# Kernel tuning notes

Hardware: AMD Instinct MI355X
Metric: run time of the kernel (lower is better)

## Reference

```python
import jax, jax.numpy as jnp
import numpy as np

HEADS = 8


def _gat(X, A, Wq, Wk, Wv, Wo, units):
    B, N, _ = X.shape
    # QKV projections -> [B, H, N, units]
    Q = (X @ Wq).reshape(B, N, HEADS, units).transpose(0, 2, 1, 3)
    K = (X @ Wk).reshape(B, N, HEADS, units).transpose(0, 2, 1, 3)
    V = (X @ Wv).reshape(B, N, HEADS, units).transpose(0, 2, 1, 3)
    scores = jnp.einsum('bhnd,bhmd->bhnm', Q, K) / jnp.sqrt(jnp.float32(units))
    # source adds A * -1e9 (masks where A == 1)
    scores = scores + A[:, None, :, :] * (-1e9)
    w = jax.nn.softmax(scores, axis=-1)  # dropout off at inference
    ctx = jnp.einsum('bhnm,bhmd->bhnd', w, V)
    ctx = ctx.transpose(0, 2, 1, 3).reshape(B, N, HEADS * units)
    return ctx @ Wo


def setup_inputs() -> dict:
    key = jax.random.key(0)
    ks = jax.random.split(key, 16)
    B, N, F = 8, 1024, 64
    u1, u2 = 128, 64
    g = lambda k, s: (jax.random.normal(k, s, dtype=jnp.float32)
                      * np.sqrt(2.0 / (s[0] + s[-1])).astype(np.float32))
    X = jax.random.normal(ks[0], (B, N, F), dtype=jnp.float32)
    A = jax.random.bernoulli(ks[1], 0.5, (B, N, N)).astype(jnp.float32)
    return {
        'X': X, 'A': A,
        'Wq1': g(ks[2], (F, u1 * HEADS)), 'Wk1': g(ks[3], (F, u1 * HEADS)),
        'Wv1': g(ks[4], (F, u1 * HEADS)), 'Wo1': g(ks[5], (u1 * HEADS, u1)),
        'Wq2': g(ks[6], (u1, u2 * HEADS)), 'Wk2': g(ks[7], (u1, u2 * HEADS)),
        'Wv2': g(ks[8], (u1, u2 * HEADS)), 'Wo2': g(ks[9], (u2 * HEADS, u2)),
        'W1': g(ks[10], (u2, 32)), 'b1': jnp.zeros((32,), jnp.float32),
        'W2': g(ks[11], (32, 16)), 'b2': jnp.zeros((16,), jnp.float32),
        'W3': g(ks[12], (16, 1)), 'b3': jnp.zeros((1,), jnp.float32),
    }


def reference(X, A, Wq1, Wk1, Wv1, Wo1, Wq2, Wk2, Wv2, Wo2,
              W1, b1, W2, b2, W3, b3):
    h = _gat(X, A, Wq1, Wk1, Wv1, Wo1, 128)   # [B, N, 128]
    h = _gat(h, A, Wq2, Wk2, Wv2, Wo2, 64)    # [B, N, 64]
    h = jnp.mean(h, axis=1)                   # [B, 64]
    h = jax.nn.relu(h @ W1 + b1)
    h = jax.nn.relu(h @ W2 + b2)
    return h @ W3 + b3                        # [B, 1]
```

## Files before the change

kernel.cpp:

```cpp
#include <hip/hip_runtime.h>
#include <hip/hip_bf16.h>
#include <math.h>

#define NB 8
#define NN 1024
#define NH 8

typedef __attribute__((ext_vector_type(8))) short bf16x8;
typedef __attribute__((ext_vector_type(4))) float f32x4;
typedef unsigned int u32;
typedef unsigned short u16;

__device__ __forceinline__ u16 f2bf(float f) {
    union { float f; u32 u; } v; v.f = f;
    const u32 u = v.u;
    return (u16)((u + 0x7fffu + ((u >> 16) & 1u)) >> 16);
}

__device__ __forceinline__ u32 cvt_pk_bf16(float lo, float hi) {
    u32 r;
    asm("v_cvt_pk_bf16_f32 %0, %1, %2" : "=v"(r) : "v"(lo), "v"(hi));
    return r;
}

__global__ __launch_bounds__(256) void mask_bits(const float* __restrict__ A,
                                                 u32* __restrict__ bits) {
    const int row = blockIdx.x;
    const int tid = threadIdx.x;
    const int lane = tid & 63;
    const float* __restrict__ ar = A + (size_t)row * NN;
#pragma unroll
    for (int it = 0; it < 4; ++it) {
        const int i = it * 256 + tid;
        const unsigned long long bal = __ballot(ar[i] != 0.0f);
        const int w0 = (it * 256 + (tid & ~63)) >> 5;
        if (lane == 0)  bits[(size_t)row * 32 + w0]     = (u32)bal;
        if (lane == 32) bits[(size_t)row * 32 + w0 + 1] = (u32)(bal >> 32);
    }
}

__global__ __launch_bounds__(256)
void cvt_bf16(const float* __restrict__ in, u16* __restrict__ out) {
    const int i = blockIdx.x * 256 + threadIdx.x;
    const float4 a = ((const float4*)in)[2 * i];
    const float4 b = ((const float4*)in)[2 * i + 1];
    u16 t[8] = {f2bf(a.x), f2bf(a.y), f2bf(a.z), f2bf(a.w),
                f2bf(b.x), f2bf(b.y), f2bf(b.z), f2bf(b.w)};
    ((uint4*)out)[i] = *(uint4*)t;
}

template <int KIN, int HD>
__global__ __launch_bounds__(256)
void cvt_qkvT(const float* __restrict__ Wq, const float* __restrict__ Wk,
              const float* __restrict__ Wv, u16* __restrict__ WT) {
    const int idx = blockIdx.x * 256 + threadIdx.x;
    const int c  = idx / (KIN / 8);
    const int f0 = (idx % (KIN / 8)) * 8;
    const float* __restrict__ W = (c < HD) ? Wq : (c < 2 * HD) ? Wk : Wv;
    const int cc = c % HD;
    u16 tmp[8];
#pragma unroll
    for (int j = 0; j < 8; ++j)
        tmp[j] = f2bf(W[(size_t)(f0 + j) * HD + cc]);
    *(uint4*)&WT[(size_t)c * KIN + f0] = *(uint4*)tmp;
}

template <int CIN, int COUT>
__global__ __launch_bounds__(256)
void cvt_woT(const float* __restrict__ Wo, u16* __restrict__ WoT) {
    const int idx = blockIdx.x * 256 + threadIdx.x;
    const int n  = idx / (CIN / 8);
    const int k0 = (idx % (CIN / 8)) * 8;
    u16 tmp[8];
#pragma unroll
    for (int j = 0; j < 8; ++j)
        tmp[j] = f2bf(Wo[(size_t)(k0 + j) * COUT + n]);
    *(uint4*)&WoT[(size_t)n * CIN + k0] = *(uint4*)tmp;
}

template <int KIN, int HD, int D>
__global__ __launch_bounds__(256)
void proj_mfma(const u16* __restrict__ Xb,
               const u16* __restrict__ WT,
               u16* __restrict__ Qb,
               u16* __restrict__ Kb,
               u16* __restrict__ VT,
               const float qscale) {
    constexpr int NKT = KIN / 32;
    constexpr int NTW = (3 * HD / 16) / 4;

    const int tid  = threadIdx.x;
    const int w    = tid >> 6;
    const int lane = tid & 63;
    const int g    = lane >> 4;
    const int q16  = lane & 15;
    const int r0   = blockIdx.x * 16;
    const int b    = r0 >> 10;
    const int n0   = r0 & 1023;
    const int ch   = n0 >> 5;
    const int grp  = (n0 >> 4) & 1;

    bf16x8 af[NKT];
#pragma unroll
    for (int t = 0; t < NKT; ++t)
        af[t] = *(const bf16x8*)&Xb[(size_t)(r0 + q16) * KIN + t * 32 + g * 8];

#pragma unroll 1
    for (int i = 0; i < NTW; ++i) {
        const int nt = w + 4 * i;
        const int c0 = nt * 16;
        f32x4 acc = (f32x4)0.f;
#pragma unroll
        for (int t = 0; t < NKT; ++t) {
            const bf16x8 wf = *(const bf16x8*)&WT[(size_t)(c0 + q16) * KIN + t * 32 + g * 8];
            acc = __builtin_amdgcn_mfma_f32_16x16x32_bf16(af[t], wf, acc, 0, 0, 0);
        }

        const int wcl = c0 / HD;
        const int cc  = c0 % HD;
        const int h   = cc / D;
        const int d0  = cc % D;
        const int bh  = b * NH + h;

        if (wcl == 2) {
            u16 tmp[4];
#pragma unroll
            for (int r = 0; r < 4; ++r) tmp[r] = f2bf(acc[r]);
            *(uint2*)&VT[(((size_t)bh * 32 + ch) * D + d0 + q16) * 32
                         + 8 * g + 4 * grp] = *(uint2*)tmp;
        } else {
            u16* __restrict__ O = wcl ? Kb : Qb;
            const float sc = wcl ? 1.0f : qscale;
#pragma unroll
            for (int r = 0; r < 4; ++r)
                O[((size_t)bh * NN + n0 + 4 * g + r) * D + d0 + q16] = f2bf(acc[r] * sc);
        }
    }
}

template <int D>
__global__ __launch_bounds__(256, 2)
void attn_v10(const u16* __restrict__ Qb,
              const u16* __restrict__ Kb,
              const u16* __restrict__ VT,
              const u32* __restrict__ bits,
              u16* __restrict__ Ob) {
    constexpr int ND4 = D / 32;
    constexpr int NDT = D / 16;
    constexpr int KROWB = 2 * D;
    constexpr int KBYTES = 32 * KROWB;
    constexpr int VBYTES = D * 80;

    const int tid  = threadIdx.x;
    const int w    = tid >> 6;
    const int lane = tid & 63;
    const int g    = lane >> 4;
    const int q16  = lane & 15;

    const int xcd    = blockIdx.x & 7;
    const int within = blockIdx.x >> 3;
    const int bh     = xcd * 8 + (within >> 3);
    const int b      = bh >> 3, h = bh & 7;
    const int q0     = ((within & 7) * 4 + w) * 32;

    const u16* __restrict__ qbase = Qb + (size_t)bh * NN * D;
    const u16* __restrict__ kbase = Kb + (size_t)bh * NN * D;
    const u16* __restrict__ vbase = VT + (size_t)bh * 32 * D * 32;
    const u32* __restrict__ brow0 = bits + ((size_t)b * NN + q0 + q16) * 32;
    const u32* __restrict__ brow1 = brow0 + 16 * 32;

    __shared__ alignas(16) char KsB[2][KBYTES];
    __shared__ alignas(16) char VsB[2][VBYTES];

    bool doK, doV;
    int kRow = 0, kA = 0, vD = 0, vHalf = 0;
    if constexpr (D == 128) {
        doK = true; doV = true;
        kRow = tid >> 3; kA = tid & 7;
        vD = tid >> 1;  vHalf = tid & 1;
    } else {
        doK = (tid < 128); doV = !doK;
        kRow = tid >> 2; kA = tid & 3;
        const int vt = tid - 128;
        vD = vt >> 1;   vHalf = vt & 1;
    }

    bf16x8 qf[2][ND4];
#pragma unroll
    for (int qs = 0; qs < 2; ++qs)
#pragma unroll
        for (int f = 0; f < ND4; ++f)
            qf[qs][f] = *(const bf16x8*)
                &qbase[(size_t)(q0 + qs * 16 + q16) * D + f * 32 + g * 8];

    f32x4 acc[2][NDT];
#pragma unroll
    for (int qs = 0; qs < 2; ++qs)
#pragma unroll
        for (int dt = 0; dt < NDT; ++dt) acc[qs][dt] = (f32x4)0.f;
    float l0 = 0.f, l1 = 0.f;

    uint4 sk0, sk1, sv0, sv1;
    auto stage_load = [&](int ch) {
        if (doK) {
            const u16* src = kbase + (size_t)(ch * 32 + kRow) * D + kA * 16;
            sk0 = *(const uint4*)(src);
            sk1 = *(const uint4*)(src + 8);
        }
        if (doV) {
            const u16* src = vbase + ((size_t)ch * D + vD) * 32 + vHalf * 16;
            sv0 = *(const uint4*)(src);
            sv1 = *(const uint4*)(src + 8);
        }
    };
    auto stage_write = [&](int buf) {
        if (doK) {
            char* kr = KsB[buf] + kRow * KROWB;
            *(uint4*)(kr + (((2 * kA)     ^ (kRow & 7)) * 16)) = sk0;
            *(uint4*)(kr + (((2 * kA + 1) ^ (kRow & 7)) * 16)) = sk1;
        }
        if (doV) {
            char* vr = VsB[buf] + vD * 80 + vHalf * 32;
            *(uint4*)(vr)      = sv0;
            *(uint4*)(vr + 16) = sv1;
        }
    };

    stage_load(0);
    stage_write(0);
    stage_load(1);
    __syncthreads();

#pragma unroll 1
    for (int ch = 0; ch < 32; ++ch) {
        const int cur = ch & 1;
        if (ch + 1 < 32) stage_write(cur ^ 1);
        if (ch + 2 < 32) stage_load(ch + 2);

        const u32 bw0 = brow0[ch];
        const u32 bw1 = brow1[ch];

        bf16x8 kf[2][ND4];
#pragma unroll
        for (int kb = 0; kb < 2; ++kb)
#pragma unroll
            for (int f = 0; f < ND4; ++f)
                kf[kb][f] = *(const bf16x8*)
                    (KsB[cur] + (kb * 16 + q16) * KROWB + (((f * 4 + g) ^ (q16 & 7)) * 16));

        f32x4 sA0 = (f32x4)0.f, sA1 = (f32x4)0.f;
        f32x4 sB0 = (f32x4)0.f, sB1 = (f32x4)0.f;
#pragma unroll
        for (int f = 0; f < ND4; ++f) {
            sA0 = __builtin_amdgcn_mfma_f32_16x16x32_bf16(kf[0][f], qf[0][f], sA0, 0, 0, 0);
            sA1 = __builtin_amdgcn_mfma_f32_16x16x32_bf16(kf[1][f], qf[0][f], sA1, 0, 0, 0);
            sB0 = __builtin_amdgcn_mfma_f32_16x16x32_bf16(kf[0][f], qf[1][f], sB0, 0, 0, 0);
            sB1 = __builtin_amdgcn_mfma_f32_16x16x32_bf16(kf[1][f], qf[1][f], sB1, 0, 0, 0);
        }

        bf16x8 vf[NDT];
#pragma unroll
        for (int dt = 0; dt < NDT; ++dt)
            vf[dt] = *(const bf16x8*)(VsB[cur] + (dt * 16 + q16) * 80 + g * 16);

        const u32 sh0 = bw0 >> (g * 4);
        const u32 sh1 = bw1 >> (g * 4);
        float pA0[4], pA1[4], pB0[4], pB1[4];
#pragma unroll
        for (int r = 0; r < 4; ++r) {
            const float eA0 = exp2f(sA0[r]), eA1 = exp2f(sA1[r]);
            const float eB0 = exp2f(sB0[r]), eB1 = exp2f(sB1[r]);
            pA0[r] = ((sh0 >> r) & 1u)        ? 0.f : eA0;
            pA1[r] = ((sh0 >> (16 + r)) & 1u) ? 0.f : eA1;
            pB0[r] = ((sh1 >> r) & 1u)        ? 0.f : eB0;
            pB1[r] = ((sh1 >> (16 + r)) & 1u) ? 0.f : eB1;
        }
        l0 += ((pA0[0] + pA0[1]) + (pA0[2] + pA0[3]))
            + ((pA1[0] + pA1[1]) + (pA1[2] + pA1[3]));
        l1 += ((pB0[0] + pB0[1]) + (pB0[2] + pB0[3]))
            + ((pB1[0] + pB1[1]) + (pB1[2] + pB1[3]));

        union { u32 u[4]; bf16x8 v; } paA, paB;
        paA.u[0] = cvt_pk_bf16(pA0[0], pA0[1]);
        paA.u[1] = cvt_pk_bf16(pA0[2], pA0[3]);
        paA.u[2] = cvt_pk_bf16(pA1[0], pA1[1]);
        paA.u[3] = cvt_pk_bf16(pA1[2], pA1[3]);
        paB.u[0] = cvt_pk_bf16(pB0[0], pB0[1]);
        paB.u[1] = cvt_pk_bf16(pB0[2], pB0[3]);
        paB.u[2] = cvt_pk_bf16(pB1[0], pB1[1]);
        paB.u[3] = cvt_pk_bf16(pB1[2], pB1[3]);

#pragma unroll
        for (int dt = 0; dt < NDT; ++dt) {
            acc[0][dt] = __builtin_amdgcn_mfma_f32_16x16x32_bf16(paA.v, vf[dt], acc[0][dt], 0, 0, 0);
            acc[1][dt] = __builtin_amdgcn_mfma_f32_16x16x32_bf16(paB.v, vf[dt], acc[1][dt], 0, 0, 0);
        }

        __syncthreads();
    }

#pragma unroll
    for (int qs = 0; qs < 2; ++qs) {
        float l = qs ? l1 : l0;
        l += __shfl_xor(l, 16);
        l += __shfl_xor(l, 32);
        const float inv = 1.0f / l;
        float ivr[4];
#pragma unroll
        for (int r = 0; r < 4; ++r) ivr[r] = __shfl(inv, g * 4 + r);
#pragma unroll
        for (int dt = 0; dt < NDT; ++dt)
#pragma unroll
            for (int r = 0; r < 4; ++r) {
                const int q = q0 + qs * 16 + g * 4 + r;
                Ob[(((size_t)b * NN + q) * NH + h) * D + dt * 16 + q16] =
                    f2bf(acc[qs][dt][r] * ivr[r]);
            }
    }
}

template <int CIN, int COUT, bool BF16OUT>
__global__ __launch_bounds__(256)
void wo_mfma(const u16* __restrict__ ctxb,
             const u16* __restrict__ WoT,
             void* __restrict__ Hout) {
    constexpr int NTW = COUT / 64;
    const int tid  = threadIdx.x;
    const int w    = tid >> 6;
    const int lane = tid & 63;
    const int g    = lane >> 4;
    const int q16  = lane & 15;
    const int r0   = blockIdx.x * 16;

    f32x4 acc[NTW];
#pragma unroll
    for (int nt = 0; nt < NTW; ++nt) acc[nt] = (f32x4)0.f;

    const u16* __restrict__ arow = ctxb + (size_t)(r0 + q16) * CIN + g * 8;

#pragma unroll 4
    for (int k0 = 0; k0 < CIN; k0 += 32) {
        const bf16x8 af = *(const bf16x8*)(arow + k0);
#pragma unroll
        for (int nt = 0; nt < NTW; ++nt) {
            const int n = (w * NTW + nt) * 16 + q16;
            const bf16x8 wf = *(const bf16x8*)&WoT[(size_t)n * CIN + k0 + g * 8];
            acc[nt] = __builtin_amdgcn_mfma_f32_16x16x32_bf16(af, wf, acc[nt], 0, 0, 0);
        }
    }

#pragma unroll
    for (int nt = 0; nt < NTW; ++nt)
#pragma unroll
        for (int r = 0; r < 4; ++r) {
            const size_t off = (size_t)(r0 + 4 * g + r) * COUT + (w * NTW + nt) * 16 + q16;
            if constexpr (BF16OUT) ((u16*)Hout)[off] = f2bf(acc[nt][r]);
            else                   ((float*)Hout)[off] = acc[nt][r];
        }
}

__global__ __launch_bounds__(256)
void pool_partial(const float* __restrict__ H2, float* __restrict__ partial) {
    const int b  = blockIdx.x >> 5;
    const int ch = blockIdx.x & 31;
    const int tid = threadIdx.x;
    const int o = tid & 63;
    const int g = tid >> 6;

    __shared__ float red[4][64];
    float acc = 0.f;
#pragma unroll
    for (int i = 0; i < 8; ++i) {
        const int n = ch * 32 + g * 8 + i;
        acc += H2[((size_t)b * NN + n) * 64 + o];
    }
    red[g][o] = acc;
    __syncthreads();
    if (g == 0)
        partial[((size_t)b * 32 + ch) * 64 + o] =
            (red[0][o] + red[1][o]) + (red[2][o] + red[3][o]);
}

__global__ __launch_bounds__(256)
void pool_mlp2(const float* __restrict__ partial,
               const float* __restrict__ W1, const float* __restrict__ b1,
               const float* __restrict__ W2, const float* __restrict__ b2,
               const float* __restrict__ W3, const float* __restrict__ b3,
               float* __restrict__ out) {
    const int b = blockIdx.x;
    const int tid = threadIdx.x;
    const int o = tid & 63;
    const int g = tid >> 6;
    __shared__ float red[4][64];
    __shared__ float mean[64];
    __shared__ float h1[32];
    __shared__ float h2[16];

    float acc = 0.f;
#pragma unroll
    for (int c = 0; c < 8; ++c)
        acc += partial[((size_t)b * 32 + g * 8 + c) * 64 + o];
    red[g][o] = acc;
    __syncthreads();
    if (g == 0)
        mean[o] = ((red[0][o] + red[1][o]) + (red[2][o] + red[3][o])) * (1.0f / 1024.0f);
    __syncthreads();

    if (tid < 32) {
        float a = b1[tid];
#pragma unroll
        for (int f = 0; f < 64; ++f) a = fmaf(mean[f], W1[f * 32 + tid], a);
        h1[tid] = fmaxf(a, 0.f);
    }
    __syncthreads();
    if (tid < 16) {
        float a = b2[tid];
#pragma unroll
        for (int f = 0; f < 32; ++f) a = fmaf(h1[f], W2[f * 16 + tid], a);
        h2[tid] = fmaxf(a, 0.f);
    }
    __syncthreads();
    if (tid == 0) {
        float a = b3[0];
#pragma unroll
        for (int f = 0; f < 16; ++f) a = fmaf(h2[f], W3[f], a);
        out[b] = a;
    }
}

extern "C" void kernel_launch(void* const* d_in, const int* in_sizes, int n_in,
                              void* d_out, int out_size, void* d_ws, size_t ws_size,
                              hipStream_t stream) {
    const float* X   = (const float*)d_in[0];
    const float* A   = (const float*)d_in[1];
    const float* Wq1 = (const float*)d_in[2];
    const float* Wk1 = (const float*)d_in[3];
    const float* Wv1 = (const float*)d_in[4];
    const float* Wo1 = (const float*)d_in[5];
    const float* Wq2 = (const float*)d_in[6];
    const float* Wk2 = (const float*)d_in[7];
    const float* Wv2 = (const float*)d_in[8];
    const float* Wo2 = (const float*)d_in[9];
    const float* W1  = (const float*)d_in[10];
    const float* b1  = (const float*)d_in[11];
    const float* W2  = (const float*)d_in[12];
    const float* b2  = (const float*)d_in[13];
    const float* W3  = (const float*)d_in[14];
    const float* b3  = (const float*)d_in[15];
    float* out = (float*)d_out;

    u32* bits   = (u32*)d_ws;
    u16* base   = (u16*)(bits + 262144);
    u16* Qb1    = base;  base += 8388608;
    u16* Kb1    = base;  base += 8388608;
    u16* VT1    = base;  base += 8388608;
    u16* ctx1b  = base;  base += 8388608;
    u16* WoT1   = base;  base += 131072;
    u16* Qb2    = base;  base += 4194304;
    u16* Kb2    = base;  base += 4194304;
    u16* VT2    = base;  base += 4194304;
    u16* ctx2b  = base;  base += 4194304;
    u16* WoT2   = base;  base += 32768;
    u16* Xb     = base;  base += 524288;
    u16* WqkvT1 = base;  base += 196608;
    u16* WqkvT2 = base;  base += 196608;
    u16* H1b    = base;  base += 1048576;
    float* H2   = (float*)base;
    float* partial = H2 + 524288;

    const int ROWS = NB * NN;
    const float LOG2E = 1.4426950408889634f;

    mask_bits<<<ROWS, 256, 0, stream>>>(A, bits);
    cvt_bf16<<<ROWS * 64 / 8 / 256, 256, 0, stream>>>(X, Xb);
    cvt_qkvT<64, 1024><<<3072 * 64 / 8 / 256, 256, 0, stream>>>(Wq1, Wk1, Wv1, WqkvT1);
    cvt_qkvT<128, 512><<<1536 * 128 / 8 / 256, 256, 0, stream>>>(Wq2, Wk2, Wv2, WqkvT2);
    cvt_woT<1024, 128><<<128 * 1024 / 8 / 256, 256, 0, stream>>>(Wo1, WoT1);
    cvt_woT<512, 64><<<64 * 512 / 8 / 256, 256, 0, stream>>>(Wo2, WoT2);

    proj_mfma<64, 1024, 128><<<ROWS / 16, 256, 0, stream>>>(
        Xb, WqkvT1, Qb1, Kb1, VT1, 0.08838834764831845f * LOG2E);
    attn_v10<128><<<512, 256, 0, stream>>>(Qb1, Kb1, VT1, bits, ctx1b);
    wo_mfma<1024, 128, true><<<ROWS / 16, 256, 0, stream>>>(ctx1b, WoT1, H1b);

    proj_mfma<128, 512, 64><<<ROWS / 16, 256, 0, stream>>>(
        H1b, WqkvT2, Qb2, Kb2, VT2, 0.125f * LOG2E);
    attn_v10<64><<<512, 256, 0, stream>>>(Qb2, Kb2, VT2, bits, ctx2b);
    wo_mfma<512, 64, false><<<ROWS / 16, 256, 0, stream>>>(ctx2b, WoT2, H2);

    pool_partial<<<256, 256, 0, stream>>>(H2, partial);
    pool_mlp2<<<NB, 256, 0, stream>>>(partial, W1, b1, W2, b2, W3, b3, out);
}
```

Baseline: 218.8 us.

## Widen attention key chunk to 64, compute row sums via MFMA, add setprio

Each attention loop iteration now processes 64 keys instead of 32, halving the iteration and barrier count and doubling the LDS staging buffers. The softmax denominator is accumulated with an extra MFMA against a vector of ones, which replaces the scalar adds and the final cross-lane shuffles. The MFMA phases are wrapped in s_setprio to favour matrix issue across waves. The larger LDS footprint and higher register pressure may reduce occupancy under the two-blocks-per-CU launch bound. Summing bf16-rounded probabilities also changes numerics slightly.

```diff
diff --git a/kernel.cpp b/kernel.cpp
--- a/kernel.cpp
+++ b/kernel.cpp
@@ -140,7 +140,7 @@
 
 template <int D>
 __global__ __launch_bounds__(256, 2)
-void attn_v10(const u16* __restrict__ Qb,
+void attn_v11(const u16* __restrict__ Qb,
               const u16* __restrict__ Kb,
               const u16* __restrict__ VT,
               const u32* __restrict__ bits,
@@ -148,8 +148,9 @@
     constexpr int ND4 = D / 32;
     constexpr int NDT = D / 16;
     constexpr int KROWB = 2 * D;
-    constexpr int KBYTES = 32 * KROWB;
-    constexpr int VBYTES = D * 80;
+    constexpr int KBYTES = 64 * KROWB;
+    constexpr int VROWB = 144;
+    constexpr int VBYTES = D * VROWB;
 
     const int tid  = threadIdx.x;
     const int w    = tid >> 6;
@@ -173,16 +174,15 @@
     __shared__ alignas(16) char VsB[2][VBYTES];
 
     bool doK, doV;
-    int kRow = 0, kA = 0, vD = 0, vHalf = 0;
+    int kRow = 0, kU0 = 0, vD = 0, vHalf = 0;
     if constexpr (D == 128) {
         doK = true; doV = true;
-        kRow = tid >> 3; kA = tid & 7;
-        vD = tid >> 1;  vHalf = tid & 1;
+        kRow = tid >> 2;           kU0 = (tid & 3) * 4;
+        vD   = tid >> 1;           vHalf = tid & 1;
     } else {
         doK = (tid < 128); doV = !doK;
-        kRow = tid >> 2; kA = tid & 3;
-        const int vt = tid - 128;
-        vD = vt >> 1;   vHalf = vt & 1;
+        kRow = (tid & 127) >> 1;   kU0 = (tid & 1) * 4;
+        vD   = (tid & 127) >> 1;   vHalf = tid & 1;
     }
 
     bf16x8 qf[2][ND4];
@@ -194,35 +194,48 @@
                 &qbase[(size_t)(q0 + qs * 16 + q16) * D + f * 32 + g * 8];
 
     f32x4 acc[2][NDT];
-#pragma unroll
-    for (int qs = 0; qs < 2; ++qs)
+    f32x4 accL[2];
+#pragma unroll
+    for (int qs = 0; qs < 2; ++qs) {
+        accL[qs] = (f32x4)0.f;
 #pragma unroll
         for (int dt = 0; dt < NDT; ++dt) acc[qs][dt] = (f32x4)0.f;
-    float l0 = 0.f, l1 = 0.f;
-
-    uint4 sk0, sk1, sv0, sv1;
+    }
+
+    const short oneb = (short)0x3F80;
+    const bf16x8 ones = {oneb, oneb, oneb, oneb, oneb, oneb, oneb, oneb};
+
+    uint4 skr0, skr1, skr2, skr3, svr0, svr1, svr2, svr3;
     auto stage_load = [&](int ch) {
         if (doK) {
-            const u16* src = kbase + (size_t)(ch * 32 + kRow) * D + kA * 16;
-            sk0 = *(const uint4*)(src);
-            sk1 = *(const uint4*)(src + 8);
+            const u16* src = kbase + (size_t)(ch * 64 + kRow) * D + kU0 * 8;
+            skr0 = *(const uint4*)(src);
+            skr1 = *(const uint4*)(src + 8);
+            skr2 = *(const uint4*)(src + 16);
+            skr3 = *(const uint4*)(src + 24);
         }
         if (doV) {
-            const u16* src = vbase + ((size_t)ch * D + vD) * 32 + vHalf * 16;
-            sv0 = *(const uint4*)(src);
-            sv1 = *(const uint4*)(src + 8);
+            const u16* src = vbase + ((size_t)(ch * 2 + vHalf) * D + vD) * 32;
+            svr0 = *(const uint4*)(src);
+            svr1 = *(const uint4*)(src + 8);
+            svr2 = *(const uint4*)(src + 16);
+            svr3 = *(const uint4*)(src + 24);
         }
     };
     auto stage_write = [&](int buf) {
         if (doK) {
             char* kr = KsB[buf] + kRow * KROWB;
-            *(uint4*)(kr + (((2 * kA)     ^ (kRow & 7)) * 16)) = sk0;
-            *(uint4*)(kr + (((2 * kA + 1) ^ (kRow & 7)) * 16)) = sk1;
+            *(uint4*)(kr + (((kU0 + 0) ^ (kRow & 7)) * 16)) = skr0;
+            *(uint4*)(kr + (((kU0 + 1) ^ (kRow & 7)) * 16)) = skr1;
+            *(uint4*)(kr + (((kU0 + 2) ^ (kRow & 7)) * 16)) = skr2;
+            *(uint4*)(kr + (((kU0 + 3) ^ (kRow & 7)) * 16)) = skr3;
         }
         if (doV) {
-            char* vr = VsB[buf] + vD * 80 + vHalf * 32;
-            *(uint4*)(vr)      = sv0;
-            *(uint4*)(vr + 16) = sv1;
+            char* vr = VsB[buf] + vD * VROWB + vHalf * 64;
+            *(uint4*)(vr)      = svr0;
+            *(uint4*)(vr + 16) = svr1;
+            *(uint4*)(vr + 32) = svr2;
+            *(uint4*)(vr + 48) = svr3;
         }
     };
 
@@ -232,82 +245,84 @@
     __syncthreads();
 
 #pragma unroll 1
-    for (int ch = 0; ch < 32; ++ch) {
+    for (int ch = 0; ch < 16; ++ch) {
         const int cur = ch & 1;
-        if (ch + 1 < 32) stage_write(cur ^ 1);
-        if (ch + 2 < 32) stage_load(ch + 2);
-
-        const u32 bw0 = brow0[ch];
-        const u32 bw1 = brow1[ch];
-
-        bf16x8 kf[2][ND4];
-#pragma unroll
-        for (int kb = 0; kb < 2; ++kb)
+        if (ch + 1 < 16) stage_write(cur ^ 1);
+        if (ch + 2 < 16) stage_load(ch + 2);
+
+        const uint2 bwA = *(const uint2*)(brow0 + ch * 2);
+        const uint2 bwB = *(const uint2*)(brow1 + ch * 2);
+
+        f32x4 s[2][4];
+#pragma unroll
+        for (int qs = 0; qs < 2; ++qs)
+#pragma unroll
+            for (int kb = 0; kb < 4; ++kb) s[qs][kb] = (f32x4)0.f;
+
+        __builtin_amdgcn_s_setprio(1);
+#pragma unroll
+        for (int kb = 0; kb < 4; ++kb) {
+            bf16x8 kf[ND4];
 #pragma unroll
             for (int f = 0; f < ND4; ++f)
-                kf[kb][f] = *(const bf16x8*)
+                kf[f] = *(const bf16x8*)
                     (KsB[cur] + (kb * 16 + q16) * KROWB + (((f * 4 + g) ^ (q16 & 7)) * 16));
-
-        f32x4 sA0 = (f32x4)0.f, sA1 = (f32x4)0.f;
-        f32x4 sB0 = (f32x4)0.f, sB1 = (f32x4)0.f;
-#pragma unroll
-        for (int f = 0; f < ND4; ++f) {
-            sA0 = __builtin_amdgcn_mfma_f32_16x16x32_bf16(kf[0][f], qf[0][f], sA0, 0, 0, 0);
-            sA1 = __builtin_amdgcn_mfma_f32_16x16x32_bf16(kf[1][f], qf[0][f], sA1, 0, 0, 0);
-            sB0 = __builtin_amdgcn_mfma_f32_16x16x32_bf16(kf[0][f], qf[1][f], sB0, 0, 0, 0);
-            sB1 = __builtin_amdgcn_mfma_f32_16x16x32_bf16(kf[1][f], qf[1][f], sB1, 0, 0, 0);
-        }
-
-        bf16x8 vf[NDT];
-#pragma unroll
-        for (int dt = 0; dt < NDT; ++dt)
-            vf[dt] = *(const bf16x8*)(VsB[cur] + (dt * 16 + q16) * 80 + g * 16);
-
-        const u32 sh0 = bw0 >> (g * 4);
-        const u32 sh1 = bw1 >> (g * 4);
-        float pA0[4], pA1[4], pB0[4], pB1[4];
-#pragma unroll
-        for (int r = 0; r < 4; ++r) {
-            const float eA0 = exp2f(sA0[r]), eA1 = exp2f(sA1[r]);
-            const float eB0 = exp2f(sB0[r]), eB1 = exp2f(sB1[r]);
-            pA0[r] = ((sh0 >> r) & 1u)        ? 0.f : eA0;
-            pA1[r] = ((sh0 >> (16 + r)) & 1u) ? 0.f : eA1;
-            pB0[r] = ((sh1 >> r) & 1u)        ? 0.f : eB0;
-            pB1[r] = ((sh1 >> (16 + r)) & 1u) ? 0.f : eB1;
-        }
-        l0 += ((pA0[0] + pA0[1]) + (pA0[2] + pA0[3]))
-            + ((pA1[0] + pA1[1]) + (pA1[2] + pA1[3]));
-        l1 += ((pB0[0] + pB0[1]) + (pB0[2] + pB0[3]))
-            + ((pB1[0] + pB1[1]) + (pB1[2] + pB1[3]));
-
-        union { u32 u[4]; bf16x8 v; } paA, paB;
-        paA.u[0] = cvt_pk_bf16(pA0[0], pA0[1]);
-        paA.u[1] = cvt_pk_bf16(pA0[2], pA0[3]);
-        paA.u[2] = cvt_pk_bf16(pA1[0], pA1[1]);
-        paA.u[3] = cvt_pk_bf16(pA1[2], pA1[3]);
-        paB.u[0] = cvt_pk_bf16(pB0[0], pB0[1]);
-        paB.u[1] = cvt_pk_bf16(pB0[2], pB0[3]);
-        paB.u[2] = cvt_pk_bf16(pB1[0], pB1[1]);
-        paB.u[3] = cvt_pk_bf16(pB1[2], pB1[3]);
-
-#pragma unroll
-        for (int dt = 0; dt < NDT; ++dt) {
-            acc[0][dt] = __builtin_amdgcn_mfma_f32_16x16x32_bf16(paA.v, vf[dt], acc[0][dt], 0, 0, 0);
-            acc[1][dt] = __builtin_amdgcn_mfma_f32_16x16x32_bf16(paB.v, vf[dt], acc[1][dt], 0, 0, 0);
-        }
+#pragma unroll
+            for (int f = 0; f < ND4; ++f) {
+                s[0][kb] = __builtin_amdgcn_mfma_f32_16x16x32_bf16(kf[f], qf[0][f], s[0][kb], 0, 0, 0);
+                s[1][kb] = __builtin_amdgcn_mfma_f32_16x16x32_bf16(kf[f], qf[1][f], s[1][kb], 0, 0, 0);
+            }
+        }
+        __builtin_amdgcn_s_setprio(0);
+
+        bf16x8 vf[2][NDT];
+#pragma unroll
+        for (int kg = 0; kg < 2; ++kg)
+#pragma unroll
+            for (int dt = 0; dt < NDT; ++dt)
+                vf[kg][dt] = *(const bf16x8*)
+                    (VsB[cur] + (dt * 16 + q16) * VROWB + kg * 64 + g * 16);
+
+        union { u32 u[4]; bf16x8 v; } pa[2][2];
+#pragma unroll
+        for (int qs = 0; qs < 2; ++qs) {
+            const u32 w0 = qs ? bwB.x : bwA.x;
+            const u32 w1 = qs ? bwB.y : bwA.y;
+#pragma unroll
+            for (int kb = 0; kb < 4; ++kb) {
+                const u32 sh = ((kb >> 1) ? w1 : w0) >> (g * 4 + (kb & 1) * 16);
+                float p[4];
+#pragma unroll
+                for (int r = 0; r < 4; ++r) {
+                    const float e = exp2f(s[qs][kb][r]);
+                    p[r] = ((sh >> r) & 1u) ? 0.f : e;
+                }
+                pa[qs][kb >> 1].u[(kb & 1) * 2 + 0] = cvt_pk_bf16(p[0], p[1]);
+                pa[qs][kb >> 1].u[(kb & 1) * 2 + 1] = cvt_pk_bf16(p[2], p[3]);
+            }
+        }
+
+        __builtin_amdgcn_s_setprio(1);
+#pragma unroll
+        for (int kg = 0; kg < 2; ++kg) {
+            accL[0] = __builtin_amdgcn_mfma_f32_16x16x32_bf16(pa[0][kg].v, ones, accL[0], 0, 0, 0);
+            accL[1] = __builtin_amdgcn_mfma_f32_16x16x32_bf16(pa[1][kg].v, ones, accL[1], 0, 0, 0);
+#pragma unroll
+            for (int dt = 0; dt < NDT; ++dt) {
+                acc[0][dt] = __builtin_amdgcn_mfma_f32_16x16x32_bf16(pa[0][kg].v, vf[kg][dt], acc[0][dt], 0, 0, 0);
+                acc[1][dt] = __builtin_amdgcn_mfma_f32_16x16x32_bf16(pa[1][kg].v, vf[kg][dt], acc[1][dt], 0, 0, 0);
+            }
+        }
+        __builtin_amdgcn_s_setprio(0);
 
         __syncthreads();
     }
 
 #pragma unroll
     for (int qs = 0; qs < 2; ++qs) {
-        float l = qs ? l1 : l0;
-        l += __shfl_xor(l, 16);
-        l += __shfl_xor(l, 32);
-        const float inv = 1.0f / l;
         float ivr[4];
 #pragma unroll
-        for (int r = 0; r < 4; ++r) ivr[r] = __shfl(inv, g * 4 + r);
+        for (int r = 0; r < 4; ++r) ivr[r] = 1.0f / accL[qs][r];
 #pragma unroll
         for (int dt = 0; dt < NDT; ++dt)
 #pragma unroll
@@ -480,12 +495,12 @@
 
     proj_mfma<64, 1024, 128><<<ROWS / 16, 256, 0, stream>>>(
         Xb, WqkvT1, Qb1, Kb1, VT1, 0.08838834764831845f * LOG2E);
-    attn_v10<128><<<512, 256, 0, stream>>>(Qb1, Kb1, VT1, bits, ctx1b);
+    attn_v11<128><<<512, 256, 0, stream>>>(Qb1, Kb1, VT1, bits, ctx1b);
     wo_mfma<1024, 128, true><<<ROWS / 16, 256, 0, stream>>>(ctx1b, WoT1, H1b);
 
     proj_mfma<128, 512, 64><<<ROWS / 16, 256, 0, stream>>>(
         H1b, WqkvT2, Qb2, Kb2, VT2, 0.125f * LOG2E);
-    attn_v10<64><<<512, 256, 0, stream>>>(Qb2, Kb2, VT2, bits, ctx2b);
+    attn_v11<64><<<512, 256, 0, stream>>>(Qb2, Kb2, VT2, bits, ctx2b);
     wo_mfma<512, 64, false><<<ROWS / 16, 256, 0, stream>>>(ctx2b, WoT2, H2);
 
     pool_partial<<<256, 256, 0, stream>>>(H2, partial);
```

New measurement: 212.9 us (median of 2 runs). 2.7% less time.
